# Kernel optimization log

Hardware: AMD Instinct MI355X
Metric: run time of the kernel (lower is better)

The kernel has to match this reference:

```python
import jax, jax.numpy as jnp
import numpy as np

DIM = 192; HEADS = 6
RES = (8, 96, 180)      # (Pl, Lat, Lon), all divisible by window -> pad/crop are no-ops
WIN = (2, 6, 12)        # (win_pl, win_lat, win_lon)
SHIFT = (1, 3, 6)
MLP_RATIO = 4


def earth_position_index(win):
    wpl, wlat, wlon = win
    zi = np.arange(wpl); zj = -np.arange(wpl) * wpl
    hi = np.arange(wlat); hj = -np.arange(wlat) * wlat
    w = np.arange(wlon)
    c1 = np.stack(np.meshgrid(zi, hi, w, indexing='ij')).reshape(3, -1)
    c2 = np.stack(np.meshgrid(zj, hj, w, indexing='ij')).reshape(3, -1)
    coords = (c1[:, :, None] - c2[:, None, :]).transpose(1, 2, 0).copy()  # (N, N, 3)
    coords[:, :, 2] += wlon - 1
    coords[:, :, 1] *= 2 * wlon - 1
    coords[:, :, 0] *= (2 * wlon - 1) * wlat * wlat
    return coords.sum(-1)  # (N, N) int index into bias table


def shift_window_mask(res, win, shift):
    Pl, Lat, Lon = res; wpl, wlat, wlon = win; spl, slat, slon = shift
    m = np.zeros((Pl, Lat, Lon + slon))
    cnt = 0
    pls = (slice(0, -wpl), slice(-wpl, -spl), slice(-spl, None))
    las = (slice(0, -wlat), slice(-wlat, -slat), slice(-slat, None))
    los = (slice(0, -wlon), slice(-wlon, -slon), slice(-slon, None))
    for p in pls:
        for l in las:
            for o in los:
                m[p, l, o] = cnt; cnt += 1
    m = m[:, :, :Lon]
    npl, nlat, nlon = Pl // wpl, Lat // wlat, Lon // wlon
    mw = m.reshape(npl, wpl, nlat, wlat, nlon, wlon).transpose(4, 0, 2, 1, 3, 5)
    mw = mw.reshape(nlon, npl * nlat, wpl * wlat * wlon)
    am = mw[:, :, None, :] - mw[:, :, :, None]
    return np.where(am != 0, -100.0, 0.0).astype(np.float32)  # (nlon, nW, N, N)


EPI = earth_position_index(WIN)                       # static int index
ATTN_MASK = shift_window_mask(RES, WIN, SHIFT)        # static float mask


def setup_inputs() -> dict:
    key = jax.random.key(0)
    ks = jax.random.split(key, 16)
    Pl, Lat, Lon = RES; wpl, wlat, wlon = WIN
    L = Pl * Lat * Lon
    nW = (Pl // wpl) * (Lat // wlat)  # type_of_windows
    tbl = wpl ** 2 * wlat ** 2 * (2 * wlon - 1)
    C = DIM; H = MLP_RATIO * DIM
    n = lambda k, s, std=0.02: (jax.random.normal(k, s, dtype=jnp.float32) * std)
    return {
        'x': jax.random.normal(ks[0], (1, L, C), dtype=jnp.float32),
        'norm1_g': jnp.ones((C,), jnp.float32), 'norm1_b': jnp.zeros((C,), jnp.float32),
        'qkv_w': n(ks[1], (C, 3 * C)), 'qkv_b': jnp.zeros((3 * C,), jnp.float32),
        'bias_table': n(ks[2], (tbl, nW, HEADS)),
        'proj_w': n(ks[3], (C, C)), 'proj_b': jnp.zeros((C,), jnp.float32),
        'norm2_g': jnp.ones((C,), jnp.float32), 'norm2_b': jnp.zeros((C,), jnp.float32),
        'fc1_w': n(ks[4], (C, H)), 'fc1_b': jnp.zeros((H,), jnp.float32),
        'fc2_w': n(ks[5], (H, C)), 'fc2_b': jnp.zeros((C,), jnp.float32),
    }


def _layernorm(y, g, b, eps=1e-5):
    mu = y.mean(-1, keepdims=True)
    var = y.var(-1, keepdims=True)
    return (y - mu) / jnp.sqrt(var + eps) * g + b


def reference(x, norm1_g, norm1_b, qkv_w, qkv_b, bias_table, proj_w, proj_b,
              norm2_g, norm2_b, fc1_w, fc1_b, fc2_w, fc2_b):
    B, L, C = x.shape
    Pl, Lat, Lon = RES; wpl, wlat, wlon = WIN; spl, slat, slon = SHIFT
    npl, nlat, nlon = Pl // wpl, Lat // wlat, Lon // wlon
    N = wpl * wlat * wlon; nW = npl * nlat
    h = HEADS; d = C // h
    scale = d ** -0.5

    shortcut = x
    y = _layernorm(x, norm1_g, norm1_b).reshape(B, Pl, Lat, Lon, C)
    y = jnp.roll(y, shift=(-spl, -slat, -slon), axis=(1, 2, 3))
    # window partition: b (npl wpl)(nlat wlat)(nlon wlon) c -> (b nlon)(npl nlat)(wpl wlat wlon) c
    yw = y.reshape(B, npl, wpl, nlat, wlat, nlon, wlon, C)
    yw = yw.transpose(0, 5, 1, 3, 2, 4, 6, 7).reshape(B * nlon, nW, N, C)

    qkv = (yw @ qkv_w + qkv_b).reshape(B * nlon, nW, N, 3, h, d)
    qkv = qkv.transpose(3, 0, 4, 1, 2, 5)  # (3, B_, h, nW, N, d)
    q, k, v = qkv[0] * scale, qkv[1], qkv[2]
    attn = jnp.einsum('bhwnd,bhwmd->bhwnm', q, k)  # (B_, h, nW, N, N)

    bias = bias_table[EPI.reshape(-1)].reshape(N, N, nW, h).transpose(3, 2, 0, 1)  # (h, nW, N, N)
    attn = attn + bias[None]
    mask = jnp.asarray(ATTN_MASK)  # (nlon, nW, N, N)
    attn = attn.reshape(B, nlon, h, nW, N, N) + mask[None, :, None]
    attn = jax.nn.softmax(attn.reshape(B * nlon, h, nW, N, N), axis=-1)

    out = jnp.einsum('bhwnm,bhwmd->bhwnd', attn, v)
    out = out.transpose(0, 2, 3, 1, 4).reshape(B * nlon, nW, N, C)
    out = out @ proj_w + proj_b
    # window reverse + un-shift
    out = out.reshape(B, nlon, npl, nlat, wpl, wlat, wlon, C)
    out = out.transpose(0, 2, 4, 3, 5, 1, 6, 7).reshape(B, Pl, Lat, Lon, C)
    out = jnp.roll(out, shift=(spl, slat, slon), axis=(1, 2, 3)).reshape(B, L, C)

    x = shortcut + out
    y = _layernorm(x, norm2_g, norm2_b)
    y = jax.nn.gelu(y @ fc1_w + fc1_b, approximate=False) @ fc2_w + fc2_b
    return x + y
```

## Files before the change

kernel.cpp:

```cpp
#include <hip/hip_runtime.h>


typedef __attribute__((ext_vector_type(8))) short short8;
typedef __attribute__((ext_vector_type(4))) short short4v;
typedef __attribute__((ext_vector_type(4))) float floatx4;
typedef unsigned short bfu;

#define GLOAD_LDS16(g, l)                                            \
  __builtin_amdgcn_global_load_lds(                                  \
      (const __attribute__((address_space(1))) unsigned int*)(g),    \
      (__attribute__((address_space(3))) unsigned int*)(l), 16, 0, 0)

__device__ __forceinline__ bfu f2bf(float f) {
  unsigned int u = __builtin_bit_cast(unsigned int, f);
  u += 0x7fffu + ((u >> 16) & 1u);
  return (bfu)(u >> 16);
}
__device__ __forceinline__ float bf2f(bfu s) {
  return __builtin_bit_cast(float, (unsigned int)s << 16);
}

__global__ void wt_kernel(const float* __restrict__ src, bfu* __restrict__ dst,
                          int K, int N) {
  int idx = blockIdx.x * 256 + threadIdx.x;
  if (idx >= K * N) return;
  int k = idx / N, n = idx % N;
  dst[(size_t)n * K + k] = f2bf(src[idx]);
}

__global__ void bias2_kernel(const float* __restrict__ table,
                             bfu* __restrict__ out) {
  int idx = blockIdx.x * 256 + threadIdx.x;
  if (idx >= 1271808) return;
  int h = idx / 211968;
  int r = idx % 211968;
  int w = r / 3312, ep = r % 3312;
  out[idx] = f2bf(table[(size_t)ep * 384 + w * 6 + h] * 1.4426950408889634f);
}

__global__ void vpad_kernel(unsigned int* __restrict__ vbw) {
  int tid = threadIdx.x;
  int dd = tid >> 3, c = tid & 7;
  vbw[(size_t)blockIdx.x * 2560 + dd * 80 + 72 + c] = 0;
}

__global__ __launch_bounds__(256) void ln1_kernel(
    const float* __restrict__ x, const float* __restrict__ g,
    const float* __restrict__ be, bfu* __restrict__ A1) {
  int wv = threadIdx.x >> 6, lane = threadIdx.x & 63;
  int r = blockIdx.x * 4 + wv;
  int n = r % 144, w = (r / 144) & 63, bb = r / 9216;
  int ip = w >> 4, il = w & 15;
  int p1 = n / 72, rem = n % 72, l1 = rem / 12, o1 = rem % 12;
  int pl = ip * 2 + p1 + 1;   if (pl >= 8) pl -= 8;
  int lat = il * 6 + l1 + 3;  if (lat >= 96) lat -= 96;
  int lon = bb * 12 + o1 + 6; if (lon >= 180) lon -= 180;
  size_t t = (size_t)(pl * 96 + lat) * 180 + lon;
  const float* xr = x + t * 192;
  float v0 = xr[lane], v1 = xr[lane + 64], v2 = xr[lane + 128];
  float s = v0 + v1 + v2;
  #pragma unroll
  for (int o = 32; o; o >>= 1) s += __shfl_xor(s, o);
  float mu = s * (1.0f / 192.0f);
  float d0 = v0 - mu, d1 = v1 - mu, d2 = v2 - mu;
  float q2 = d0 * d0 + d1 * d1 + d2 * d2;
  #pragma unroll
  for (int o = 32; o; o >>= 1) q2 += __shfl_xor(q2, o);
  float rstd = rsqrtf(q2 * (1.0f / 192.0f) + 1e-5f);
  bfu* orow = A1 + (size_t)r * 192;
  orow[lane]       = f2bf(d0 * rstd * g[lane]       + be[lane]);
  orow[lane + 64]  = f2bf(d1 * rstd * g[lane + 64]  + be[lane + 64]);
  orow[lane + 128] = f2bf(d2 * rstd * g[lane + 128] + be[lane + 128]);
}

__global__ __launch_bounds__(256) void ln2_kernel(
    const float* __restrict__ xin, const float* __restrict__ g,
    const float* __restrict__ be, bfu* __restrict__ yout) {
  int wv = threadIdx.x >> 6, lane = threadIdx.x & 63;
  size_t r = (size_t)blockIdx.x * 4 + wv;
  const float* xr = xin + r * 192;
  float v0 = xr[lane], v1 = xr[lane + 64], v2 = xr[lane + 128];
  float s = v0 + v1 + v2;
  #pragma unroll
  for (int o = 32; o; o >>= 1) s += __shfl_xor(s, o);
  float mu = s * (1.0f / 192.0f);
  float d0 = v0 - mu, d1 = v1 - mu, d2 = v2 - mu;
  float q2 = d0 * d0 + d1 * d1 + d2 * d2;
  #pragma unroll
  for (int o = 32; o; o >>= 1) q2 += __shfl_xor(q2, o);
  float rstd = rsqrtf(q2 * (1.0f / 192.0f) + 1e-5f);
  bfu* orow = yout + r * 192;
  orow[lane]       = f2bf(d0 * rstd * g[lane]       + be[lane]);
  orow[lane + 64]  = f2bf(d1 * rstd * g[lane + 64]  + be[lane + 64]);
  orow[lane + 128] = f2bf(d2 * rstd * g[lane + 128] + be[lane + 128]);
}

__global__ __launch_bounds__(256, 3) void gemm_kernel(
    const bfu* __restrict__ A, const bfu* __restrict__ BT,
    const float* __restrict__ bias, int K, int NT, int mode,
    const float* aux, void* out0, void* out1, void* out2) {
  __shared__ __align__(16) short Bs[18432];
  bfu* E = (bfu*)Bs;
  const int tid = threadIdx.x;
  const int wv = tid >> 6, lane = tid & 63;
  const int r16 = lane & 15, quad = lane >> 4;
  const int sw = r16 & 7;

  const int W = gridDim.x;
  const int work = (blockIdx.x & 7) * (W >> 3) + (blockIdx.x >> 3);
  const int m0 = (work / NT) * 128;
  const int n0 = (work % NT) * 96;
  const bfu* Bsrc = BT + (size_t)n0 * K;

  const short* Arow[2];
  #pragma unroll
  for (int s = 0; s < 2; ++s)
    Arow[s] = (const short*)A + (size_t)(m0 + wv * 32 + s * 16 + r16) * K + quad * 8;

  floatx4 acc[2][6];
  #pragma unroll
  for (int s = 0; s < 2; ++s)
    #pragma unroll
    for (int j = 0; j < 6; ++j) acc[s][j] = (floatx4){0.f, 0.f, 0.f, 0.f};

  for (int kc = 0; kc < K; kc += 192) {
    __syncthreads();
    #pragma unroll
    for (int j = 0; j < 9; ++j) {
      int c = j * 256 + tid;
      int row = c / 24, sl = c % 24;
      int l = (sl & ~7) | ((sl ^ row) & 7);
      GLOAD_LDS16(Bsrc + (size_t)row * K + kc + l * 8, Bs + c * 8);
    }
    short8 ar[2][6];
    #pragma unroll
    for (int s = 0; s < 2; ++s)
      #pragma unroll
      for (int ks = 0; ks < 6; ++ks)
        ar[s][ks] = *(const short8*)(Arow[s] + kc + ks * 32);
    __syncthreads();
    #pragma unroll
    for (int ks = 0; ks < 6; ++ks) {
      const int s_log = ks * 4 + quad;
      const int p8 = ((s_log & ~7) | ((s_log ^ sw) & 7)) * 8;
      short8 b[6];
      #pragma unroll
      for (int j = 0; j < 6; ++j)
        b[j] = *(const short8*)(Bs + (j * 16 + r16) * 192 + p8);
      #pragma unroll
      for (int j = 0; j < 6; ++j) {
        acc[0][j] = __builtin_amdgcn_mfma_f32_16x16x32_bf16(ar[0][ks], b[j], acc[0][j], 0, 0, 0);
        acc[1][j] = __builtin_amdgcn_mfma_f32_16x16x32_bf16(ar[1][ks], b[j], acc[1][j], 0, 0, 0);
      }
    }
  }

  if (mode == 0 || mode == 2) {
    __syncthreads();
    #pragma unroll
    for (int s = 0; s < 2; ++s) {
      int er = wv * 32 + s * 16 + quad * 4;
      #pragma unroll
      for (int j = 0; j < 6; ++j) {
        int c = j * 16 + r16;
        float bia = bias[n0 + c];
        #pragma unroll
        for (int i = 0; i < 4; ++i) {
          float val = acc[s][j][i] + bia;
          if (mode == 0) {
            if (n0 < 192) val *= 0.25503633958871686f;
            E[(er + i) * 104 + c] = f2bf(val);
          } else {
            float ge = 0.5f * val * (1.0f + erff(val * 0.70710678118654752f));
            E[(er + i) * 104 + c] = f2bf(ge);
          }
        }
      }
    }
    __syncthreads();
    if (mode == 2) {
      #pragma unroll
      for (int u = 0; u < 6; ++u) {
        int id = u * 256 + tid;
        int r = id / 12, c8 = (id % 12) * 8;
        *(short8*)((bfu*)out0 + (size_t)(m0 + r) * 768 + n0 + c8) =
            *(const short8*)(E + r * 104 + c8);
      }
    } else if (n0 < 384) {
      bfu* dst = (bfu*)(n0 < 192 ? out0 : out1);
      #pragma unroll
      for (int u = 0; u < 6; ++u) {
        int id = u * 256 + tid;
        int r = id / 12, c8 = (id % 12) * 8;
        int row = m0 + r;
        int n = row % 144, w = (row / 144) & 63, bb = row / 9216;
        int head = ((n0 + c8) % 192) >> 5, dd = c8 & 31;
        size_t win = (size_t)(bb * 6 + head) * 64 + w;
        *(short8*)(dst + win * 4608 + n * 32 + dd) =
            *(const short8*)(E + r * 104 + c8);
      }
    } else {
      #pragma unroll
      for (int u = 0; u < 6; ++u) {
        int id = u * 256 + tid;
        int c = id % 96, k8 = id / 96;
        int r0 = k8 * 8;
        int row0 = m0 + r0;
        int n = row0 % 144, w = (row0 / 144) & 63, bb = row0 / 9216;
        int head = ((n0 + c) % 192) >> 5, dd = c & 31;
        size_t win = (size_t)(bb * 6 + head) * 64 + w;
        short8 t8;
        #pragma unroll
        for (int i = 0; i < 8; ++i) t8[i] = (short)E[(r0 + i) * 104 + c];
        *(short8*)((bfu*)out2 + win * 5120 + dd * 160 + n) = t8;
      }
    }
  } else {
    #pragma unroll
    for (int s = 0; s < 2; ++s) {
      const int row0 = m0 + wv * 32 + s * 16 + quad * 4;
      #pragma unroll
      for (int j = 0; j < 6; ++j) {
        int col = n0 + j * 16 + r16;
        float bia = bias[col];
        #pragma unroll
        for (int i = 0; i < 4; ++i) {
          int row = row0 + i;
          float val = acc[s][j][i] + bia;
          if (mode == 1) {
            int n = row % 144, w = (row / 144) & 63, bb = row / 9216;
            int ip = w >> 4, il = w & 15;
            int p1 = n / 72, rem = n % 72, l1 = rem / 12, o1 = rem % 12;
            int pl = ip * 2 + p1 + 1;   if (pl >= 8) pl -= 8;
            int lat = il * 6 + l1 + 3;  if (lat >= 96) lat -= 96;
            int lon = bb * 12 + o1 + 6; if (lon >= 180) lon -= 180;
            size_t t = (size_t)(pl * 96 + lat) * 180 + lon;
            ((float*)out0)[t * 192 + col] = aux[t * 192 + col] + val;
          } else {
            size_t idx = (size_t)row * 192 + col;
            ((float*)out0)[idx] = aux[idx] + val;
          }
        }
      }
    }
  }
}

__global__ __launch_bounds__(256) void attn_kernel(
    const bfu* __restrict__ qg_, const bfu* __restrict__ kg_,
    const bfu* __restrict__ vg_, const bfu* __restrict__ tblT,
    bfu* __restrict__ aout) {
  __shared__ __align__(16) bfu Ss[144 * 148];
  __shared__ __align__(16) bfu bias_l[3312];
  __shared__ unsigned short rn[144];
  __shared__ short cm[144];
  __shared__ unsigned char regs[144];

  const int w = blockIdx.x, h0 = blockIdx.y * 2, b = blockIdx.z;
  const int tid = threadIdx.x;
  const int wv = tid >> 6, lane = tid & 63, r16 = lane & 15, quad = lane >> 4;

  if (tid < 144) {
    int n = tid;
    int p1 = n / 72, rem = n % 72, l1 = rem / 12, o1 = rem % 12;
    rn[n] = (unsigned short)(828 * p1 + 23 * l1 + o1 + 11);
    cm[n] = (short)(1656 * p1 + 138 * l1 - o1);
    int ip = w >> 4, il = w & 15;
    int pl = ip * 2 + p1, lat = il * 6 + l1, lon = b * 12 + o1;
    int rp = pl < 6 ? 0 : (pl < 7 ? 1 : 2);
    int rl = lat < 90 ? 0 : (lat < 93 ? 1 : 2);
    int ro = lon < 174 ? 0 : 1;
    regs[n] = (unsigned char)(rp * 9 + rl * 3 + ro);
  }

  {
    const bfu* bsrc = tblT + (size_t)(h0 * 64 + w) * 3312;
    GLOAD_LDS16(bsrc + tid * 8, bias_l + tid * 8);
    if (tid < 158) GLOAD_LDS16(bsrc + (256 + tid) * 8, bias_l + (256 + tid) * 8);
  }
  __syncthreads();

  short cmv[9];
  unsigned char creg[9];
  #pragma unroll
  for (int j = 0; j < 9; ++j) {
    int c = r16 + 16 * j;
    cmv[j] = cm[c];
    creg[j] = regs[c];
  }

  short4v ov[2][5];
  #pragma unroll
  for (int hh = 0; hh < 2; ++hh) {
    const int h = h0 + hh;
    const size_t win = (size_t)((b * 6 + h) * 64 + w);
    const bfu* qg = qg_ + win * 4608;
    const bfu* kg = kg_ + win * 4608;
    const bfu* vt = vg_ + win * 5120;

    short8 qf[9];
    #pragma unroll
    for (int t9 = 0; t9 < 9; ++t9)
      qf[t9] = *(const short8*)(qg + (t9 * 16 + r16) * 32 + quad * 8);
    const int tma = wv * 2, tmb = wv * 2 + 1;
    short8 kfa = *(const short8*)(kg + (tma * 16 + r16) * 32 + quad * 8);
    short8 kfb = *(const short8*)(kg + (tmb * 16 + r16) * 32 + quad * 8);
    short8 kfc = *(const short8*)(kg + (128 + r16) * 32 + quad * 8);
    const floatx4 z = (floatx4){0.f, 0.f, 0.f, 0.f};
    #pragma unroll
    for (int tn = 0; tn < 9; ++tn) {
      bfu* srow = Ss + (tn * 16 + quad * 4) * 148;
      floatx4 d = __builtin_amdgcn_mfma_f32_16x16x32_bf16(qf[tn], kfa, z, 0, 0, 0);
      #pragma unroll
      for (int i = 0; i < 4; ++i) srow[i * 148 + tma * 16 + r16] = f2bf(d[i]);
      d = __builtin_amdgcn_mfma_f32_16x16x32_bf16(qf[tn], kfb, z, 0, 0, 0);
      #pragma unroll
      for (int i = 0; i < 4; ++i) srow[i * 148 + tmb * 16 + r16] = f2bf(d[i]);
      if ((tn & 3) == wv) {
        d = __builtin_amdgcn_mfma_f32_16x16x32_bf16(qf[tn], kfc, z, 0, 0, 0);
        #pragma unroll
        for (int i = 0; i < 4; ++i) srow[i * 148 + 128 + r16] = f2bf(d[i]);
      }
    }
    __syncthreads();

    for (int rb = 0; rb < 9; ++rb) {
      int rr = rb * 16 + wv * 4 + quad;
      unsigned char rgn = regs[rr];
      int rnv = rn[rr];
      const bfu* srow = Ss + rr * 148;
      float v[9];
      float sum = 0.f;
      #pragma unroll
      for (int j = 0; j < 9; ++j) {
        float s = bf2f(srow[r16 + 16 * j]) + bf2f(bias_l[rnv + cmv[j]]);
        s = (creg[j] != rgn) ? s - 144.26950408889634f : s;
        v[j] = exp2f(s);
        sum += v[j];
      }
      #pragma unroll
      for (int o = 8; o; o >>= 1) sum += __shfl_xor(sum, o);
      float inv = 1.0f / sum;
      bfu* wrow = Ss + rr * 148;
      #pragma unroll
      for (int j = 0; j < 9; ++j) wrow[r16 + 16 * j] = f2bf(v[j] * inv);
    }
    __syncthreads();

    if (hh == 0) {
      const bfu* bsrc = tblT + (size_t)((h0 + 1) * 64 + w) * 3312;
      GLOAD_LDS16(bsrc + tid * 8, bias_l + tid * 8);
      if (tid < 158) GLOAD_LDS16(bsrc + (256 + tid) * 8, bias_l + (256 + tid) * 8);
    }

    short8 bfr[2][5];
    #pragma unroll
    for (int td = 0; td < 2; ++td)
      #pragma unroll
      for (int km = 0; km < 5; ++km)
        bfr[td][km] =
            *(const short8*)(vt + (td * 16 + r16) * 160 + km * 32 + quad * 8);

    #pragma unroll
    for (int u = 0; u < 5; ++u) {
      int t = wv * 5 + u;
      if (t < 18) {
        int tn = t >> 1, td = t & 1;
        floatx4 acc = (floatx4){0.f, 0.f, 0.f, 0.f};
        #pragma unroll
        for (int km = 0; km < 5; ++km) {
          short8 a;
          if (km == 4 && quad >= 2) {
            a = (short8)(short)0;
          } else {
            const bfu* ap = Ss + (tn * 16 + r16) * 148 + km * 32 + quad * 8;
            *(short4v*)&a       = *(const short4v*)ap;
            *((short4v*)&a + 1) = *(const short4v*)(ap + 4);
          }
          acc = __builtin_amdgcn_mfma_f32_16x16x32_bf16(bfr[td][km], a, acc, 0, 0, 0);
        }
        short4v o;
        #pragma unroll
        for (int i = 0; i < 4; ++i) o[i] = (short)f2bf(acc[i]);
        ov[hh][u] = o;
      }
    }
    if (hh == 0) __syncthreads();
  }

  __syncthreads();
  bfu* Os = Ss;
  #pragma unroll
  for (int u = 0; u < 5; ++u) {
    int t = wv * 5 + u;
    if (t < 18) {
      int tn = t >> 1, td = t & 1;
      int ro = tn * 16 + r16;
      *(short4v*)(Os + ro * 80 + td * 16 + quad * 4)      = ov[0][u];
      *(short4v*)(Os + ro * 80 + 32 + td * 16 + quad * 4) = ov[1][u];
    }
  }
  __syncthreads();
  const size_t obase = (size_t)((b * 64 + w) * 144) * 192 + h0 * 32;
  #pragma unroll
  for (int u = 0; u < 5; ++u) {
    int c = u * 256 + tid;
    if (c < 1152) {
      int r = c >> 3, k = c & 7;
      *(short8*)(aout + obase + (size_t)r * 192 + k * 8) =
          *(const short8*)(Os + r * 80 + k * 8);
    }
  }
}

extern "C" void kernel_launch(void* const* d_in, const int* in_sizes, int n_in,
                              void* d_out, int out_size, void* d_ws, size_t ws_size,
                              hipStream_t stream) {
  (void)in_sizes; (void)n_in; (void)out_size; (void)ws_size;
  const float* x     = (const float*)d_in[0];
  const float* n1g   = (const float*)d_in[1];
  const float* n1b   = (const float*)d_in[2];
  const float* qkvw  = (const float*)d_in[3];
  const float* qkvb  = (const float*)d_in[4];
  const float* tbl   = (const float*)d_in[5];
  const float* projw = (const float*)d_in[6];
  const float* projb = (const float*)d_in[7];
  const float* n2g   = (const float*)d_in[8];
  const float* n2b   = (const float*)d_in[9];
  const float* fc1w  = (const float*)d_in[10];
  const float* fc1b  = (const float*)d_in[11];
  const float* fc2w  = (const float*)d_in[12];
  const float* fc2b  = (const float*)d_in[13];

  char* ws = (char*)d_ws;
  bfu* wt_qkv   = (bfu*)(ws + 0);
  bfu* wt_proj  = (bfu*)(ws + 221184);
  bfu* wt_fc1   = (bfu*)(ws + 294912);
  bfu* wt_fc2   = (bfu*)(ws + 589824);
  bfu* tblT     = (bfu*)(ws + 884736);
  bfu* A1       = (bfu*)(ws + 16809984);
  bfu* qb       = (bfu*)(ws + 69894144);
  bfu* kb       = (bfu*)(ws + 122978304);
  bfu* vb       = (bfu*)(ws + 176062464);
  bfu* hb       = qb;
  float* out    = (float*)d_out;

  wt_kernel<<<432, 256, 0, stream>>>(qkvw, wt_qkv, 192, 576);
  wt_kernel<<<144, 256, 0, stream>>>(projw, wt_proj, 192, 192);
  wt_kernel<<<576, 256, 0, stream>>>(fc1w, wt_fc1, 192, 768);
  wt_kernel<<<576, 256, 0, stream>>>(fc2w, wt_fc2, 768, 192);
  bias2_kernel<<<4968, 256, 0, stream>>>(tbl, tblT);
  vpad_kernel<<<5760, 256, 0, stream>>>((unsigned int*)vb);
  ln1_kernel<<<34560, 256, 0, stream>>>(x, n1g, n1b, A1);
  gemm_kernel<<<6480, 256, 0, stream>>>(A1, wt_qkv, qkvb, 192, 6, 0,
                                        nullptr, qb, kb, vb);
  attn_kernel<<<dim3(64, 3, 15), 256, 0, stream>>>(qb, kb, vb, tblT, A1);
  gemm_kernel<<<2160, 256, 0, stream>>>(A1, wt_proj, projb, 192, 2, 1,
                                        x, out, nullptr, nullptr);
  ln2_kernel<<<34560, 256, 0, stream>>>(out, n2g, n2b, A1);
  gemm_kernel<<<8640, 256, 0, stream>>>(A1, wt_fc1, fc1b, 192, 8, 2,
                                        nullptr, hb, nullptr, nullptr);
  gemm_kernel<<<2160, 256, 0, stream>>>(hb, wt_fc2, fc2b, 768, 2, 3,
                                        out, out, nullptr, nullptr);
}
```

Measured before the change: 987.9 us.

## Shrink LDS footprint in GEMM and attention kernels to raise occupancy

The GEMM kernel now stages both A and B tiles through LDS with 64-wide K chunks, replacing the full 192-wide B tile and direct A register loads. This cuts the shared-memory footprint and raises the launch-bounds occupancy target from 3 to 4 blocks. The attention kernel processes queries in three chunks of 48 rows so the score buffer shrinks to a third of its size, and both heads' bias tables are loaded up front. The cost is more barriers and K-loop iterations in both kernels, and less data held in registers per step.

```diff
diff --git a/kernel.cpp b/kernel.cpp
--- a/kernel.cpp
+++ b/kernel.cpp
@@ -95,12 +95,14 @@
   orow[lane + 128] = f2bf(d2 * rstd * g[lane + 128] + be[lane + 128]);
 }
 
-__global__ __launch_bounds__(256, 3) void gemm_kernel(
+__global__ __launch_bounds__(256, 4) void gemm_kernel(
     const bfu* __restrict__ A, const bfu* __restrict__ BT,
     const float* __restrict__ bias, int K, int NT, int mode,
     const float* aux, void* out0, void* out1, void* out2) {
-  __shared__ __align__(16) short Bs[18432];
-  bfu* E = (bfu*)Bs;
+  __shared__ __align__(16) short LB[14336];
+  short* As = LB;
+  short* Bs = LB + 8192;
+  bfu* E = (bfu*)LB;
   const int tid = threadIdx.x;
   const int wv = tid >> 6, lane = tid & 63;
   const int r16 = lane & 15, quad = lane >> 4;
@@ -112,46 +114,43 @@
   const int n0 = (work % NT) * 96;
   const bfu* Bsrc = BT + (size_t)n0 * K;
 
-  const short* Arow[2];
+  floatx4 acc[2][6];
   #pragma unroll
   for (int s = 0; s < 2; ++s)
-    Arow[s] = (const short*)A + (size_t)(m0 + wv * 32 + s * 16 + r16) * K + quad * 8;
-
-  floatx4 acc[2][6];
-  #pragma unroll
-  for (int s = 0; s < 2; ++s)
     #pragma unroll
     for (int j = 0; j < 6; ++j) acc[s][j] = (floatx4){0.f, 0.f, 0.f, 0.f};
 
-  for (int kc = 0; kc < K; kc += 192) {
+  for (int kc = 0; kc < K; kc += 64) {
     __syncthreads();
     #pragma unroll
-    for (int j = 0; j < 9; ++j) {
+    for (int j = 0; j < 4; ++j) {
       int c = j * 256 + tid;
-      int row = c / 24, sl = c % 24;
-      int l = (sl & ~7) | ((sl ^ row) & 7);
+      int row = c >> 3, l = (c & 7) ^ (row & 7);
+      GLOAD_LDS16(A + (size_t)(m0 + row) * K + kc + l * 8, As + c * 8);
+    }
+    #pragma unroll
+    for (int j = 0; j < 3; ++j) {
+      int c = j * 256 + tid;
+      int row = c >> 3, l = (c & 7) ^ (row & 7);
       GLOAD_LDS16(Bsrc + (size_t)row * K + kc + l * 8, Bs + c * 8);
     }
-    short8 ar[2][6];
-    #pragma unroll
-    for (int s = 0; s < 2; ++s)
-      #pragma unroll
-      for (int ks = 0; ks < 6; ++ks)
-        ar[s][ks] = *(const short8*)(Arow[s] + kc + ks * 32);
     __syncthreads();
     #pragma unroll
-    for (int ks = 0; ks < 6; ++ks) {
-      const int s_log = ks * 4 + quad;
-      const int p8 = ((s_log & ~7) | ((s_log ^ sw) & 7)) * 8;
-      short8 b[6];
+    for (int ks = 0; ks < 2; ++ks) {
+      const int p8 = ((ks * 4 + quad) ^ sw) * 8;
+      short8 a[2], b[6];
+      #pragma unroll
+      for (int s = 0; s < 2; ++s)
+        a[s] = *(const short8*)(As + (wv * 32 + s * 16 + r16) * 64 + p8);
       #pragma unroll
       for (int j = 0; j < 6; ++j)
-        b[j] = *(const short8*)(Bs + (j * 16 + r16) * 192 + p8);
-      #pragma unroll
-      for (int j = 0; j < 6; ++j) {
-        acc[0][j] = __builtin_amdgcn_mfma_f32_16x16x32_bf16(ar[0][ks], b[j], acc[0][j], 0, 0, 0);
-        acc[1][j] = __builtin_amdgcn_mfma_f32_16x16x32_bf16(ar[1][ks], b[j], acc[1][j], 0, 0, 0);
-      }
+        b[j] = *(const short8*)(Bs + (j * 16 + r16) * 64 + p8);
+      #pragma unroll
+      for (int s = 0; s < 2; ++s)
+        #pragma unroll
+        for (int j = 0; j < 6; ++j)
+          acc[s][j] =
+              __builtin_amdgcn_mfma_f32_16x16x32_bf16(a[s], b[j], acc[s][j], 0, 0, 0);
     }
   }
 
@@ -250,8 +249,8 @@
     const bfu* __restrict__ qg_, const bfu* __restrict__ kg_,
     const bfu* __restrict__ vg_, const bfu* __restrict__ tblT,
     bfu* __restrict__ aout) {
-  __shared__ __align__(16) bfu Ss[144 * 148];
-  __shared__ __align__(16) bfu bias_l[3312];
+  __shared__ __align__(16) bfu Ss[48 * 148];
+  __shared__ __align__(16) bfu bias2[2 * 3312];
   __shared__ unsigned short rn[144];
   __shared__ short cm[144];
   __shared__ unsigned char regs[144];
@@ -273,10 +272,14 @@
     regs[n] = (unsigned char)(rp * 9 + rl * 3 + ro);
   }
 
-  {
-    const bfu* bsrc = tblT + (size_t)(h0 * 64 + w) * 3312;
-    GLOAD_LDS16(bsrc + tid * 8, bias_l + tid * 8);
-    if (tid < 158) GLOAD_LDS16(bsrc + (256 + tid) * 8, bias_l + (256 + tid) * 8);
+  #pragma unroll
+  for (int j = 0; j < 4; ++j) {
+    int c = j * 256 + tid;
+    if (c < 828) {
+      int hh = c / 414, cc = c - hh * 414;
+      GLOAD_LDS16(tblT + (size_t)((h0 + hh) * 64 + w) * 3312 + cc * 8,
+                  bias2 + hh * 3312 + cc * 8);
+    }
   }
   __syncthreads();
 
@@ -289,127 +292,127 @@
     creg[j] = regs[c];
   }
 
-  short4v ov[2][5];
-  #pragma unroll
-  for (int hh = 0; hh < 2; ++hh) {
-    const int h = h0 + hh;
-    const size_t win = (size_t)((b * 6 + h) * 64 + w);
-    const bfu* qg = qg_ + win * 4608;
-    const bfu* kg = kg_ + win * 4608;
-    const bfu* vt = vg_ + win * 5120;
-
-    short8 qf[9];
-    #pragma unroll
-    for (int t9 = 0; t9 < 9; ++t9)
-      qf[t9] = *(const short8*)(qg + (t9 * 16 + r16) * 32 + quad * 8);
-    const int tma = wv * 2, tmb = wv * 2 + 1;
-    short8 kfa = *(const short8*)(kg + (tma * 16 + r16) * 32 + quad * 8);
-    short8 kfb = *(const short8*)(kg + (tmb * 16 + r16) * 32 + quad * 8);
-    short8 kfc = *(const short8*)(kg + (128 + r16) * 32 + quad * 8);
-    const floatx4 z = (floatx4){0.f, 0.f, 0.f, 0.f};
-    #pragma unroll
-    for (int tn = 0; tn < 9; ++tn) {
-      bfu* srow = Ss + (tn * 16 + quad * 4) * 148;
-      floatx4 d = __builtin_amdgcn_mfma_f32_16x16x32_bf16(qf[tn], kfa, z, 0, 0, 0);
-      #pragma unroll
-      for (int i = 0; i < 4; ++i) srow[i * 148 + tma * 16 + r16] = f2bf(d[i]);
-      d = __builtin_amdgcn_mfma_f32_16x16x32_bf16(qf[tn], kfb, z, 0, 0, 0);
-      #pragma unroll
-      for (int i = 0; i < 4; ++i) srow[i * 148 + tmb * 16 + r16] = f2bf(d[i]);
-      if ((tn & 3) == wv) {
-        d = __builtin_amdgcn_mfma_f32_16x16x32_bf16(qf[tn], kfc, z, 0, 0, 0);
-        #pragma unroll
-        for (int i = 0; i < 4; ++i) srow[i * 148 + 128 + r16] = f2bf(d[i]);
-      }
-    }
+  const size_t obase = (size_t)((b * 64 + w) * 144) * 192 + h0 * 32;
+  const floatx4 z = (floatx4){0.f, 0.f, 0.f, 0.f};
+
+  #pragma unroll
+  for (int qc = 0; qc < 3; ++qc) {
+    short4v ov[2][2];
+    #pragma unroll
+    for (int hh = 0; hh < 2; ++hh) {
+      const size_t win = (size_t)((b * 6 + h0 + hh) * 64 + w);
+      const bfu* qg = qg_ + win * 4608;
+      const bfu* kg = kg_ + win * 4608;
+      const bfu* vt = vg_ + win * 5120;
+
+      short8 qf[3];
+      #pragma unroll
+      for (int t3 = 0; t3 < 3; ++t3)
+        qf[t3] = *(const short8*)(qg + ((qc * 3 + t3) * 16 + r16) * 32 + quad * 8);
+      const int tma = wv * 2, tmb = wv * 2 + 1;
+      short8 kfa = *(const short8*)(kg + (tma * 16 + r16) * 32 + quad * 8);
+      short8 kfb = *(const short8*)(kg + (tmb * 16 + r16) * 32 + quad * 8);
+      short8 kfc = *(const short8*)(kg + (128 + r16) * 32 + quad * 8);
+      #pragma unroll
+      for (int tn = 0; tn < 3; ++tn) {
+        int tng = qc * 3 + tn;
+        bfu* srow = Ss + (tn * 16 + quad * 4) * 148;
+        floatx4 d = __builtin_amdgcn_mfma_f32_16x16x32_bf16(qf[tn], kfa, z, 0, 0, 0);
+        #pragma unroll
+        for (int i = 0; i < 4; ++i) srow[i * 148 + tma * 16 + r16] = f2bf(d[i]);
+        d = __builtin_amdgcn_mfma_f32_16x16x32_bf16(qf[tn], kfb, z, 0, 0, 0);
+        #pragma unroll
+        for (int i = 0; i < 4; ++i) srow[i * 148 + tmb * 16 + r16] = f2bf(d[i]);
+        if ((tng & 3) == wv) {
+          d = __builtin_amdgcn_mfma_f32_16x16x32_bf16(qf[tn], kfc, z, 0, 0, 0);
+          #pragma unroll
+          for (int i = 0; i < 4; ++i) srow[i * 148 + 128 + r16] = f2bf(d[i]);
+        }
+      }
+      __syncthreads();
+
+      for (int rb = 0; rb < 3; ++rb) {
+        int rrl = rb * 16 + wv * 4 + quad;
+        int rrg = qc * 48 + rrl;
+        unsigned char rgn = regs[rrg];
+        int rnv = rn[rrg];
+        const bfu* srow = Ss + rrl * 148;
+        const bfu* bl = bias2 + hh * 3312;
+        float v[9];
+        float sum = 0.f;
+        #pragma unroll
+        for (int j = 0; j < 9; ++j) {
+          float s = bf2f(srow[r16 + 16 * j]) + bf2f(bl[rnv + cmv[j]]);
+          s = (creg[j] != rgn) ? s - 144.26950408889634f : s;
+          v[j] = exp2f(s);
+          sum += v[j];
+        }
+        #pragma unroll
+        for (int o = 8; o; o >>= 1) sum += __shfl_xor(sum, o);
+        float inv = 1.0f / sum;
+        bfu* wrow = Ss + rrl * 148;
+        #pragma unroll
+        for (int j = 0; j < 9; ++j) wrow[r16 + 16 * j] = f2bf(v[j] * inv);
+      }
+      __syncthreads();
+
+      short8 bfr[2][5];
+      #pragma unroll
+      for (int td = 0; td < 2; ++td)
+        #pragma unroll
+        for (int km = 0; km < 5; ++km)
+          bfr[td][km] =
+              *(const short8*)(vt + (td * 16 + r16) * 160 + km * 32 + quad * 8);
+
+      #pragma unroll
+      for (int u = 0; u < 2; ++u) {
+        int t = u * 4 + wv;
+        if (t < 6) {
+          int tn = t >> 1, td = t & 1;
+          floatx4 acc = z;
+          #pragma unroll
+          for (int km = 0; km < 5; ++km) {
+            short8 a;
+            if (km == 4 && quad >= 2) {
+              a = (short8)(short)0;
+            } else {
+              const bfu* ap = Ss + (tn * 16 + r16) * 148 + km * 32 + quad * 8;
+              *(short4v*)&a       = *(const short4v*)ap;
+              *((short4v*)&a + 1) = *(const short4v*)(ap + 4);
+            }
+            acc = __builtin_amdgcn_mfma_f32_16x16x32_bf16(bfr[td][km], a, acc, 0, 0, 0);
+          }
+          short4v o;
+          #pragma unroll
+          for (int i = 0; i < 4; ++i) o[i] = (short)f2bf(acc[i]);
+          ov[hh][u] = o;
+        }
+      }
+      __syncthreads();
+    }
+
+    #pragma unroll
+    for (int hh = 0; hh < 2; ++hh)
+      #pragma unroll
+      for (int u = 0; u < 2; ++u) {
+        int t = u * 4 + wv;
+        if (t < 6) {
+          int tn = t >> 1, td = t & 1;
+          int ro = tn * 16 + r16;
+          *(short4v*)(Ss + ro * 80 + hh * 32 + td * 16 + quad * 4) = ov[hh][u];
+        }
+      }
     __syncthreads();
-
-    for (int rb = 0; rb < 9; ++rb) {
-      int rr = rb * 16 + wv * 4 + quad;
-      unsigned char rgn = regs[rr];
-      int rnv = rn[rr];
-      const bfu* srow = Ss + rr * 148;
-      float v[9];
-      float sum = 0.f;
-      #pragma unroll
-      for (int j = 0; j < 9; ++j) {
-        float s = bf2f(srow[r16 + 16 * j]) + bf2f(bias_l[rnv + cmv[j]]);
-        s = (creg[j] != rgn) ? s - 144.26950408889634f : s;
-        v[j] = exp2f(s);
-        sum += v[j];
-      }
-      #pragma unroll
-      for (int o = 8; o; o >>= 1) sum += __shfl_xor(sum, o);
-      float inv = 1.0f / sum;
-      bfu* wrow = Ss + rr * 148;
-      #pragma unroll
-      for (int j = 0; j < 9; ++j) wrow[r16 + 16 * j] = f2bf(v[j] * inv);
-    }
-    __syncthreads();
-
-    if (hh == 0) {
-      const bfu* bsrc = tblT + (size_t)((h0 + 1) * 64 + w) * 3312;
-      GLOAD_LDS16(bsrc + tid * 8, bias_l + tid * 8);
-      if (tid < 158) GLOAD_LDS16(bsrc + (256 + tid) * 8, bias_l + (256 + tid) * 8);
-    }
-
-    short8 bfr[2][5];
-    #pragma unroll
-    for (int td = 0; td < 2; ++td)
-      #pragma unroll
-      for (int km = 0; km < 5; ++km)
-        bfr[td][km] =
-            *(const short8*)(vt + (td * 16 + r16) * 160 + km * 32 + quad * 8);
-
-    #pragma unroll
-    for (int u = 0; u < 5; ++u) {
-      int t = wv * 5 + u;
-      if (t < 18) {
-        int tn = t >> 1, td = t & 1;
-        floatx4 acc = (floatx4){0.f, 0.f, 0.f, 0.f};
-        #pragma unroll
-        for (int km = 0; km < 5; ++km) {
-          short8 a;
-          if (km == 4 && quad >= 2) {
-            a = (short8)(short)0;
-          } else {
-            const bfu* ap = Ss + (tn * 16 + r16) * 148 + km * 32 + quad * 8;
-            *(short4v*)&a       = *(const short4v*)ap;
-            *((short4v*)&a + 1) = *(const short4v*)(ap + 4);
-          }
-          acc = __builtin_amdgcn_mfma_f32_16x16x32_bf16(bfr[td][km], a, acc, 0, 0, 0);
-        }
-        short4v o;
-        #pragma unroll
-        for (int i = 0; i < 4; ++i) o[i] = (short)f2bf(acc[i]);
-        ov[hh][u] = o;
-      }
-    }
-    if (hh == 0) __syncthreads();
-  }
-
-  __syncthreads();
-  bfu* Os = Ss;
-  #pragma unroll
-  for (int u = 0; u < 5; ++u) {
-    int t = wv * 5 + u;
-    if (t < 18) {
-      int tn = t >> 1, td = t & 1;
-      int ro = tn * 16 + r16;
-      *(short4v*)(Os + ro * 80 + td * 16 + quad * 4)      = ov[0][u];
-      *(short4v*)(Os + ro * 80 + 32 + td * 16 + quad * 4) = ov[1][u];
-    }
-  }
-  __syncthreads();
-  const size_t obase = (size_t)((b * 64 + w) * 144) * 192 + h0 * 32;
-  #pragma unroll
-  for (int u = 0; u < 5; ++u) {
-    int c = u * 256 + tid;
-    if (c < 1152) {
-      int r = c >> 3, k = c & 7;
-      *(short8*)(aout + obase + (size_t)r * 192 + k * 8) =
-          *(const short8*)(Os + r * 80 + k * 8);
-    }
+    #pragma unroll
+    for (int u = 0; u < 2; ++u) {
+      int c = u * 256 + tid;
+      if (c < 384) {
+        int r = c >> 3, k = c & 7;
+        *(short8*)(aout + obase + (size_t)(qc * 48 + r) * 192 + k * 8) =
+            *(const short8*)(Ss + r * 80 + k * 8);
+      }
+    }
+    if (qc < 2) __syncthreads();
   }
 }
 
```

Result: no change. 997.0 us (+0.9%).
